# Performance work log

Hardware: AMD Instinct MI355X
Metric: run time of the kernel (lower is better)

Reference implementation:

```python
import jax, jax.numpy as jnp
import numpy as np

N = 100            # node_num
B = 8              # batch
H = 256            # node_feature_hidden_dim
FD, FL = 16, 16    # node_feature_dim, node_feature_len
OUT = 4            # edge_output_dim
E = N * (N - 1)    # 9900 directed edges (off-diagonal)
_off = np.ones((N, N)) - np.eye(N)
REC, SEND = np.where(_off)   # rel_rec one-hot rows = REC, rel_send = SEND
REC = jnp.asarray(REC, jnp.int32)
SEND = jnp.asarray(SEND, jnp.int32)
BN_EPS = 1e-5


def _mlp(x, w1, b1, w2, b2, g, beta):
    # Linear-ReLU-Linear-ReLU-BatchNorm1d (training-mode batch stats, dropout=0)
    h = jax.nn.relu(x @ w1 + b1)
    h = jax.nn.relu(h @ w2 + b2)
    b_, e_, f_ = h.shape
    hf = h.reshape(b_ * e_, f_)
    mu = hf.mean(0)
    var = hf.var(0)  # biased variance, as torch BN uses for normalization
    hn = (hf - mu) * jax.lax.rsqrt(var + BN_EPS) * g + beta
    return hn.reshape(b_, e_, f_)


def _node2edge(x):
    # gather form of rel_send @ x / rel_rec @ x, cat([senders, receivers])
    return jnp.concatenate([x[:, SEND, :], x[:, REC, :]], axis=2)


def _edge2node(x):
    # scatter form of rel_rec.T @ x; original divides by incoming.size(1) == N
    incoming = jnp.zeros((x.shape[0], N, x.shape[2]), x.dtype).at[:, REC, :].add(x)
    return incoming / N


def setup_inputs() -> dict:
    key = jax.random.key(0)
    ks = jax.random.split(key, 40)

    def rn(k, shape, s=0.05):
        return (jax.random.normal(k, shape) * s).astype(jnp.float32)

    inp = {
        'x': rn(ks[0], (B, N, FD, FL), 1.0),
        'h': rn(ks[1], (B, N, 8, 8), 1.0),
        't_nodes': N,
        't_edges': E,
        'nodes_mask': jnp.ones((N,), jnp.int32),
        'edges_mask': jnp.ones((E,), jnp.int32),
    }
    n_in = {'mlp1': FD * FL, 'mlp2': 2 * H, 'mlp3': H, 'mlp4': 3 * H}
    i = 2
    for name, nin in n_in.items():
        inp[name + '_w1'] = rn(ks[i], (nin, H)); i += 1
        inp[name + '_b1'] = jnp.full((H,), 0.1, jnp.float32)
        inp[name + '_w2'] = rn(ks[i], (H, H)); i += 1
        inp[name + '_b2'] = jnp.full((H,), 0.1, jnp.float32)
        inp[name + '_g'] = jnp.ones((H,), jnp.float32)
        inp[name + '_beta'] = jnp.zeros((H,), jnp.float32)
    inp['fc_w'] = rn(ks[i], (H, OUT)); i += 1
    inp['fc_b'] = jnp.full((OUT,), 0.1, jnp.float32)
    return inp


def reference(x, h, t_nodes, t_edges, nodes_mask, edges_mask,
              mlp1_w1, mlp1_b1, mlp1_w2, mlp1_b2, mlp1_g, mlp1_beta,
              mlp2_w1, mlp2_b1, mlp2_w2, mlp2_b2, mlp2_g, mlp2_beta,
              mlp3_w1, mlp3_b1, mlp3_w2, mlp3_b2, mlp3_g, mlp3_beta,
              mlp4_w1, mlp4_b1, mlp4_w2, mlp4_b2, mlp4_g, mlp4_beta,
              fc_w, fc_b):
    # h, t_nodes, t_edges, nodes_mask, edges_mask are unused by the original forward
    xx = x.reshape(x.shape[0], x.shape[1], -1).astype(jnp.float32)  # [B,N,FD*FL]
    xx = _mlp(xx, mlp1_w1, mlp1_b1, mlp1_w2, mlp1_b2, mlp1_g, mlp1_beta)  # [B,N,H]
    xe = _node2edge(xx)                                                   # [B,E,2H]
    xe = _mlp(xe, mlp2_w1, mlp2_b1, mlp2_w2, mlp2_b2, mlp2_g, mlp2_beta)  # [B,E,H]
    x_skip = xe
    xn = _edge2node(xe)                                                   # [B,N,H]
    xn = _mlp(xn, mlp3_w1, mlp3_b1, mlp3_w2, mlp3_b2, mlp3_g, mlp3_beta)
    xe2 = _node2edge(xn)                                                  # [B,E,2H]
    xc = jnp.concatenate([xe2, x_skip], axis=2)                           # [B,E,3H]
    xc = _mlp(xc, mlp4_w1, mlp4_b1, mlp4_w2, mlp4_b2, mlp4_g, mlp4_beta)  # [B,E,H]
    z_g = xc @ fc_w + fc_b                                                # [B,E,OUT]
    return z_g
```

## Files before the change

kernel.cpp:

```cpp
#include <hip/hip_runtime.h>
#include <hip/hip_bf16.h>

#define Nn 100
#define Bb 8
#define Hh 256
#define Ee 9900
#define RE 79200
#define RN 800
#define BN_EPS 1e-5f

typedef __attribute__((ext_vector_type(8))) unsigned short ushort8_t;
typedef __attribute__((ext_vector_type(4))) unsigned short ushort4_t;
typedef __attribute__((ext_vector_type(8))) short bf16x8;
typedef __attribute__((ext_vector_type(4))) float f32x4;

__device__ __forceinline__ float bf2f(unsigned short u){
  return __uint_as_float(((unsigned)u) << 16);
}
__device__ __forceinline__ unsigned short f2bf(float f){
  unsigned u = __float_as_uint(f);
  return (unsigned short)((u + 0x7fffu + ((u >> 16) & 1u)) >> 16);
}

__device__ __forceinline__ void affine_prologue(const float* __restrict__ stats,
    float cnt, const float* __restrict__ g, const float* __restrict__ beta,
    float* a, float* c, int tid){
  if (tid < 256){
    float inv = 1.0f / cnt;
    float mu  = stats[tid] * inv;
    float var = fmaxf(stats[256 + tid] * inv - mu * mu, 0.f);
    float aa  = g[tid] * rsqrtf(var + BN_EPS);
    a[tid] = aa;
    c[tid] = beta[tid] - mu * aa;
  }
}

__device__ __forceinline__ void affine_reg(const float* __restrict__ stats,
    float cnt, const float* __restrict__ g, const float* __restrict__ be,
    int cb, float4& av, float4& cv){
  float4 s = *(const float4*)(stats + cb);
  float4 q = *(const float4*)(stats + 256 + cb);
  float4 gg = *(const float4*)(g + cb);
  float4 bb = *(const float4*)(be + cb);
  float inv = 1.0f / cnt;
  float mx = s.x*inv, my = s.y*inv, mz = s.z*inv, mw = s.w*inv;
  av.x = gg.x * rsqrtf(fmaxf(q.x*inv - mx*mx, 0.f) + BN_EPS); cv.x = bb.x - mx*av.x;
  av.y = gg.y * rsqrtf(fmaxf(q.y*inv - my*my, 0.f) + BN_EPS); cv.y = bb.y - my*av.y;
  av.z = gg.z * rsqrtf(fmaxf(q.z*inv - mz*mz, 0.f) + BN_EPS); cv.z = bb.z - mz*av.z;
  av.w = gg.w * rsqrtf(fmaxf(q.w*inv - mw*mw, 0.f) + BN_EPS); cv.w = bb.w - mw*av.w;
}

__device__ __forceinline__ void gemm_f32(const float* IN, const float* __restrict__ W,
                                         float acc[8][4], int tr, int tc){
  for (int k = 0; k < 256; k += 4){
    float4 w0 = *(const float4*)(W + (size_t)(k+0)*256 + 4*tc);
    float4 w1 = *(const float4*)(W + (size_t)(k+1)*256 + 4*tc);
    float4 w2 = *(const float4*)(W + (size_t)(k+2)*256 + 4*tc);
    float4 w3 = *(const float4*)(W + (size_t)(k+3)*256 + 4*tc);
    #pragma unroll
    for (int rr = 0; rr < 8; rr++){
      float4 iv = *(const float4*)(IN + (tr*8+rr)*256 + k);
      acc[rr][0] += iv.x*w0.x + iv.y*w1.x + iv.z*w2.x + iv.w*w3.x;
      acc[rr][1] += iv.x*w0.y + iv.y*w1.y + iv.z*w2.y + iv.w*w3.y;
      acc[rr][2] += iv.x*w0.z + iv.y*w1.z + iv.z*w2.z + iv.w*w3.z;
      acc[rr][3] += iv.x*w0.w + iv.y*w1.w + iv.z*w2.w + iv.w*w3.w;
    }
  }
}

__device__ __forceinline__ void mfma_gemm64(const unsigned short* Alds,
    const unsigned short* __restrict__ Bf, f32x4 acc[4][4], int w, int lane){
  const int l15 = lane & 15, kg = lane >> 4;
  for (int ks = 0; ks < 8; ks++){
    bf16x8 a[4];
    #pragma unroll
    for (int rf = 0; rf < 4; rf++){
      int byte = (((rf*16 + l15)*256 + ks*32 + kg*8) * 2) ^ ((l15 & 7) << 4);
      a[rf] = *(const bf16x8*)((const char*)Alds + byte);
    }
    const unsigned short* bp = Bf + ((size_t)(ks*16 + w*4)*64 + lane)*8;
    #pragma unroll
    for (int cf = 0; cf < 4; cf++){
      bf16x8 b = *(const bf16x8*)(bp + cf*64*8);
      #pragma unroll
      for (int rf = 0; rf < 4; rf++)
        acc[rf][cf] = __builtin_amdgcn_mfma_f32_16x16x32_bf16(a[rf], b, acc[rf][cf], 0,0,0);
    }
  }
}

__device__ __forceinline__ void zero_acc4(f32x4 acc[4][4]){
  #pragma unroll
  for (int i = 0; i < 4; i++)
    #pragma unroll
    for (int j = 0; j < 4; j++){
      f32x4 z = {0.f, 0.f, 0.f, 0.f};
      acc[i][j] = z;
    }
}

#define STATS_PUSH(statsp)                                   \
  __syncthreads();                                           \
  atomicAdd(&(statsp)[tid], red[tid]);                       \
  atomicAdd(&(statsp)[tid + 256], red[tid + 256]);

__global__ void k_wprep(const float* __restrict__ W, unsigned short* __restrict__ out,
                        int ktiles){
  int id = blockIdx.x * 256 + threadIdx.x;
  int total = ktiles * 16 * 64;
  if (id >= total) return;
  int lane = id & 63, tile = id >> 6;
  int tc = tile & 15, tk = tile >> 4;
  int kbase = tk*32 + (lane>>4)*8, col = tc*16 + (lane&15);
  ushort8_t o;
  #pragma unroll
  for (int j = 0; j < 8; j++) o[j] = f2bf(W[(size_t)(kbase+j)*256 + col]);
  *(ushort8_t*)(out + (size_t)id*8) = o;
}

__global__ __launch_bounds__(256,2) void k_mlp1(
    const float* __restrict__ x,
    const float* __restrict__ W1, const float* __restrict__ b1,
    const float* __restrict__ W2, const float* __restrict__ b2,
    float* __restrict__ h1, float* __restrict__ stats){
  __shared__ float IN[32*256];
  __shared__ float O1[32*256];
  __shared__ float red[512];
  int tid = threadIdx.x, tr = tid >> 6, tc = tid & 63;
  int r0 = blockIdx.x * 32;
  #pragma unroll
  for (int j = 0; j < 8; j++){
    int idx = tid*4 + j*1024;
    *(float4*)(IN + idx) = *(const float4*)(x + (size_t)r0*256 + idx);
  }
  red[tid] = 0.f; red[tid + 256] = 0.f;
  __syncthreads();
  float acc[8][4];
  #pragma unroll
  for (int rr = 0; rr < 8; rr++){ acc[rr][0]=acc[rr][1]=acc[rr][2]=acc[rr][3]=0.f; }
  gemm_f32(IN, W1, acc, tr, tc);
  {
    float4 bb = *(const float4*)(b1 + 4*tc);
    #pragma unroll
    for (int rr = 0; rr < 8; rr++){
      float4 o;
      o.x = fmaxf(acc[rr][0]+bb.x, 0.f);
      o.y = fmaxf(acc[rr][1]+bb.y, 0.f);
      o.z = fmaxf(acc[rr][2]+bb.z, 0.f);
      o.w = fmaxf(acc[rr][3]+bb.w, 0.f);
      *(float4*)(O1 + (tr*8+rr)*256 + 4*tc) = o;
    }
  }
  __syncthreads();
  #pragma unroll
  for (int rr = 0; rr < 8; rr++){ acc[rr][0]=acc[rr][1]=acc[rr][2]=acc[rr][3]=0.f; }
  gemm_f32(O1, W2, acc, tr, tc);
  {
    float4 bb = *(const float4*)(b2 + 4*tc);
    float ls0=0,ls1=0,ls2=0,ls3=0,lq0=0,lq1=0,lq2=0,lq3=0;
    #pragma unroll
    for (int rr = 0; rr < 8; rr++){
      float4 v;
      v.x = fmaxf(acc[rr][0]+bb.x, 0.f);
      v.y = fmaxf(acc[rr][1]+bb.y, 0.f);
      v.z = fmaxf(acc[rr][2]+bb.z, 0.f);
      v.w = fmaxf(acc[rr][3]+bb.w, 0.f);
      *(float4*)(h1 + ((size_t)(r0 + tr*8 + rr))*256 + 4*tc) = v;
      ls0+=v.x; lq0+=v.x*v.x; ls1+=v.y; lq1+=v.y*v.y;
      ls2+=v.z; lq2+=v.z*v.z; ls3+=v.w; lq3+=v.w*v.w;
    }
    atomicAdd(&red[4*tc+0], ls0); atomicAdd(&red[4*tc+1], ls1);
    atomicAdd(&red[4*tc+2], ls2); atomicAdd(&red[4*tc+3], ls3);
    atomicAdd(&red[256+4*tc+0], lq0); atomicAdd(&red[256+4*tc+1], lq1);
    atomicAdd(&red[256+4*tc+2], lq2); atomicAdd(&red[256+4*tc+3], lq3);
  }
  STATS_PUSH(stats)
}

__global__ __launch_bounds__(256,2) void k_nodepq(
    const float* __restrict__ hsrc, const float* __restrict__ stats,
    const float* __restrict__ g, const float* __restrict__ be,
    const float* __restrict__ W512,
    unsigned short* __restrict__ P, unsigned short* __restrict__ Q){
  __shared__ float IN[32*256];
  int tid = threadIdx.x, tr = tid >> 6, tc = tid & 63;
  int part = blockIdx.x / 25;
  int r0 = (blockIdx.x % 25) * 32;
  int cb = (tid*4) & 255;
  float4 av, cv;
  affine_reg(stats, (float)RN, g, be, cb, av, cv);
  #pragma unroll
  for (int j = 0; j < 8; j++){
    int idx = tid*4 + j*1024;
    int row = idx >> 8;
    float4 v = *(const float4*)(hsrc + (size_t)(r0+row)*256 + cb);
    float4 o;
    o.x = v.x*av.x + cv.x; o.y = v.y*av.y + cv.y;
    o.z = v.z*av.z + cv.z; o.w = v.w*av.w + cv.w;
    *(float4*)(IN + idx) = o;
  }
  __syncthreads();
  float acc[8][4];
  #pragma unroll
  for (int rr = 0; rr < 8; rr++){ acc[rr][0]=acc[rr][1]=acc[rr][2]=acc[rr][3]=0.f; }
  gemm_f32(IN, W512 + (size_t)part*65536, acc, tr, tc);
  unsigned short* out = part ? Q : P;
  #pragma unroll
  for (int rr = 0; rr < 8; rr++){
    ushort4_t o;
    o[0]=f2bf(acc[rr][0]); o[1]=f2bf(acc[rr][1]);
    o[2]=f2bf(acc[rr][2]); o[3]=f2bf(acc[rr][3]);
    *(ushort4_t*)(out + (size_t)(r0 + tr*8 + rr)*256 + 4*tc) = o;
  }
}

__global__ __launch_bounds__(256,4) void k_mlp2(
    const unsigned short* __restrict__ P2, const unsigned short* __restrict__ Q2,
    const float* __restrict__ b1,
    const unsigned short* __restrict__ W2f, const float* __restrict__ b2,
    unsigned short* __restrict__ h2, float* __restrict__ stats2){
  __shared__ unsigned short O1[64*256];
  __shared__ float red[512];
  int tid = threadIdx.x, w = tid >> 6, lane = tid & 63;
  int l15 = lane & 15, kg = lane >> 4;
  int r0 = blockIdx.x * 64;
  red[tid] = 0.f; red[tid + 256] = 0.f;
  {
    int cb = lane * 4;
    float4 bb = *(const float4*)(b1 + cb);
    #pragma unroll
    for (int rr = 0; rr < 16; rr++){
      int rl = w*16+rr, rg = r0 + rl;
      int rgc = rg < RE ? rg : RE-1;
      int b = rgc / Ee, e = rgc - b*Ee;
      int i = e / 99, kk = e - i*99;
      int snd = kk + (kk >= i);
      ushort4_t pv = *(const ushort4_t*)(P2 + ((size_t)(b*Nn + snd))*256 + cb);
      ushort4_t qv = *(const ushort4_t*)(Q2 + ((size_t)(b*Nn + i))*256 + cb);
      ushort4_t o;
      o[0] = f2bf(fmaxf(bf2f(pv[0])+bf2f(qv[0])+bb.x, 0.f));
      o[1] = f2bf(fmaxf(bf2f(pv[1])+bf2f(qv[1])+bb.y, 0.f));
      o[2] = f2bf(fmaxf(bf2f(pv[2])+bf2f(qv[2])+bb.z, 0.f));
      o[3] = f2bf(fmaxf(bf2f(pv[3])+bf2f(qv[3])+bb.w, 0.f));
      int byte = ((rl*256 + cb)*2) ^ ((rl&7)<<4);
      *(ushort4_t*)((char*)O1 + byte) = o;
    }
  }
  __syncthreads();
  f32x4 acc2[4][4];
  zero_acc4(acc2);
  mfma_gemm64(O1, W2f, acc2, w, lane);
  {
    #pragma unroll
    for (int cf = 0; cf < 4; cf++){
      int col = w*64 + cf*16 + l15;
      float bb = b2[col];
      float ls = 0.f, lq = 0.f;
      #pragma unroll
      for (int rf = 0; rf < 4; rf++){
        #pragma unroll
        for (int r = 0; r < 4; r++){
          int row = rf*16 + kg*4 + r;
          if (r0 + row < RE){
            float v = fmaxf(acc2[rf][cf][r] + bb, 0.f);
            h2[(size_t)(r0 + row)*256 + col] = f2bf(v);
            ls += v; lq += v*v;
          }
        }
      }
      atomicAdd(&red[col], ls);
      atomicAdd(&red[256+col], lq);
    }
  }
  STATS_PUSH(stats2)
}

__global__ __launch_bounds__(256,4) void k_e2n(
    const unsigned short* __restrict__ h2, float* __restrict__ h3in){
  int m = blockIdx.x;
  int b = m / Nn, i = m - b*Nn;
  int c = threadIdx.x;
  const unsigned short* base = h2 + ((size_t)(b*Ee + i*99))*256 + c;
  float s = 0.f;
  #pragma unroll 4
  for (int j = 0; j < 99; j++) s += bf2f(base[(size_t)j*256]);
  h3in[(size_t)m*256 + c] = s;
}

__global__ __launch_bounds__(256,2) void k_mlp3(
    const float* __restrict__ h3in, const float* __restrict__ stats2,
    const float* __restrict__ g2, const float* __restrict__ be2,
    const float* __restrict__ W1, const float* __restrict__ b1,
    const float* __restrict__ W2, const float* __restrict__ b2,
    float* __restrict__ h3, float* __restrict__ stats3){
  __shared__ float IN[32*256];
  __shared__ float O1[32*256];
  __shared__ float red[512];
  __shared__ float ap[256], cp[256];
  int tid = threadIdx.x, tr = tid >> 6, lane = tid & 63, tc = lane;
  int r0 = blockIdx.x * 32;
  affine_prologue(stats2, (float)RE, g2, be2, ap, cp, tid);
  red[tid] = 0.f; red[tid + 256] = 0.f;
  __syncthreads();
  {
    int cb = lane * 4;
    float4 av = *(const float4*)(ap+cb), cv = *(const float4*)(cp+cb);
    #pragma unroll
    for (int rr = 0; rr < 8; rr++){
      int m = r0 + tr*8 + rr;
      float4 s = *(const float4*)(h3in + (size_t)m*256 + cb);
      float4 o;
      o.x = (s.x*av.x + 99.f*cv.x) * 0.01f;
      o.y = (s.y*av.y + 99.f*cv.y) * 0.01f;
      o.z = (s.z*av.z + 99.f*cv.z) * 0.01f;
      o.w = (s.w*av.w + 99.f*cv.w) * 0.01f;
      *(float4*)(IN + (tr*8+rr)*256 + cb) = o;
    }
  }
  __syncthreads();
  float acc[8][4];
  #pragma unroll
  for (int rr = 0; rr < 8; rr++){ acc[rr][0]=acc[rr][1]=acc[rr][2]=acc[rr][3]=0.f; }
  gemm_f32(IN, W1, acc, tr, tc);
  {
    float4 bb = *(const float4*)(b1 + 4*tc);
    #pragma unroll
    for (int rr = 0; rr < 8; rr++){
      float4 o;
      o.x = fmaxf(acc[rr][0]+bb.x, 0.f);
      o.y = fmaxf(acc[rr][1]+bb.y, 0.f);
      o.z = fmaxf(acc[rr][2]+bb.z, 0.f);
      o.w = fmaxf(acc[rr][3]+bb.w, 0.f);
      *(float4*)(O1 + (tr*8+rr)*256 + 4*tc) = o;
    }
  }
  __syncthreads();
  #pragma unroll
  for (int rr = 0; rr < 8; rr++){ acc[rr][0]=acc[rr][1]=acc[rr][2]=acc[rr][3]=0.f; }
  gemm_f32(O1, W2, acc, tr, tc);
  {
    float4 bb = *(const float4*)(b2 + 4*tc);
    float ls0=0,ls1=0,ls2=0,ls3=0,lq0=0,lq1=0,lq2=0,lq3=0;
    #pragma unroll
    for (int rr = 0; rr < 8; rr++){
      float4 v;
      v.x = fmaxf(acc[rr][0]+bb.x, 0.f);
      v.y = fmaxf(acc[rr][1]+bb.y, 0.f);
      v.z = fmaxf(acc[rr][2]+bb.z, 0.f);
      v.w = fmaxf(acc[rr][3]+bb.w, 0.f);
      *(float4*)(h3 + ((size_t)(r0 + tr*8 + rr))*256 + 4*tc) = v;
      ls0+=v.x; lq0+=v.x*v.x; ls1+=v.y; lq1+=v.y*v.y;
      ls2+=v.z; lq2+=v.z*v.z; ls3+=v.w; lq3+=v.w*v.w;
    }
    atomicAdd(&red[4*tc+0], ls0); atomicAdd(&red[4*tc+1], ls1);
    atomicAdd(&red[4*tc+2], ls2); atomicAdd(&red[4*tc+3], ls3);
    atomicAdd(&red[256+4*tc+0], lq0); atomicAdd(&red[256+4*tc+1], lq1);
    atomicAdd(&red[256+4*tc+2], lq2); atomicAdd(&red[256+4*tc+3], lq3);
  }
  STATS_PUSH(stats3)
}

__global__ __launch_bounds__(256,4) void k_mlp4(
    const unsigned short* __restrict__ h2,
    const float* __restrict__ stats2, const float* __restrict__ g2, const float* __restrict__ be2,
    const unsigned short* __restrict__ P4, const unsigned short* __restrict__ Q4,
    const float* __restrict__ b1,
    const unsigned short* __restrict__ Wsf,
    const unsigned short* __restrict__ W2f, const float* __restrict__ b2,
    unsigned short* __restrict__ h4, float* __restrict__ stats4){
  __shared__ unsigned short A[64*256];
  __shared__ float red[512];
  __shared__ int sIdx[64], rIdx[64];
  int tid = threadIdx.x, w = tid >> 6, lane = tid & 63;
  int l15 = lane & 15, kg = lane >> 4;
  int r0 = blockIdx.x * 64;
  red[tid] = 0.f; red[tid + 256] = 0.f;
  if (tid < 64){
    int rg = r0 + tid;
    int rgc = rg < RE ? rg : RE-1;
    int b = rgc / Ee, e = rgc - b*Ee;
    int i = e / 99, kk = e - i*99;
    int snd = kk + (kk >= i);
    sIdx[tid] = (b*Nn + snd)*256;
    rIdx[tid] = (b*Nn + i)*256;
  }
  {
    int cb = lane * 4;
    float4 av, cv;
    affine_reg(stats2, (float)RE, g2, be2, cb, av, cv);
    #pragma unroll
    for (int rr = 0; rr < 16; rr++){
      int rl = w*16+rr, rg = r0 + rl;
      int rgc = rg < RE ? rg : RE-1;
      ushort4_t hv = *(const ushort4_t*)(h2 + (size_t)rgc*256 + cb);
      ushort4_t o;
      o[0]=f2bf(bf2f(hv[0])*av.x+cv.x);
      o[1]=f2bf(bf2f(hv[1])*av.y+cv.y);
      o[2]=f2bf(bf2f(hv[2])*av.z+cv.z);
      o[3]=f2bf(bf2f(hv[3])*av.w+cv.w);
      int byte = ((rl*256 + cb)*2) ^ ((rl&7)<<4);
      *(ushort4_t*)((char*)A + byte) = o;
    }
  }
  __syncthreads();
  f32x4 acc[4][4];
  zero_acc4(acc);
  mfma_gemm64(A, Wsf, acc, w, lane);
  __syncthreads();
  unsigned short* O1 = A;
  {
    #pragma unroll
    for (int cf = 0; cf < 4; cf++){
      int col = w*64 + cf*16 + l15;
      float bb = b1[col];
      #pragma unroll
      for (int rf = 0; rf < 4; rf++){
        #pragma unroll
        for (int r = 0; r < 4; r++){
          int row = rf*16 + kg*4 + r;
          float v = acc[rf][cf][r] + bf2f(P4[sIdx[row] + col]) + bf2f(Q4[rIdx[row] + col]) + bb;
          v = fmaxf(v, 0.f);
          int byte = ((row*256 + col)*2) ^ ((row&7)<<4);
          *(unsigned short*)((char*)O1 + byte) = f2bf(v);
        }
      }
    }
  }
  __syncthreads();
  f32x4 acc2[4][4];
  zero_acc4(acc2);
  mfma_gemm64(O1, W2f, acc2, w, lane);
  {
    #pragma unroll
    for (int cf = 0; cf < 4; cf++){
      int col = w*64 + cf*16 + l15;
      float bb = b2[col];
      float ls = 0.f, lq = 0.f;
      #pragma unroll
      for (int rf = 0; rf < 4; rf++){
        #pragma unroll
        for (int r = 0; r < 4; r++){
          int row = rf*16 + kg*4 + r;
          if (r0 + row < RE){
            float v = fmaxf(acc2[rf][cf][r] + bb, 0.f);
            h4[(size_t)(r0 + row)*256 + col] = f2bf(v);
            ls += v; lq += v*v;
          }
        }
      }
      atomicAdd(&red[col], ls);
      atomicAdd(&red[256+col], lq);
    }
  }
  STATS_PUSH(stats4)
}

__global__ __launch_bounds__(256,2) void k_out(
    const unsigned short* __restrict__ h4, const float* __restrict__ stats4,
    const float* __restrict__ g4, const float* __restrict__ be4,
    const float* __restrict__ fcw, const float* __restrict__ fcb,
    float* __restrict__ out){
  __shared__ unsigned short T[64*264];
  __shared__ float a4[256], c4[256], Wl[1024];
  int tid = threadIdx.x;
  affine_prologue(stats4, (float)RE, g4, be4, a4, c4, tid);
  #pragma unroll
  for (int j = 0; j < 4; j++){ int id = tid + j*256; Wl[id] = fcw[id]; }
  int r0 = blockIdx.x * 64;
  #pragma unroll
  for (int j = 0; j < 8; j++){
    int flat = tid + j*256;
    int rl = flat >> 5, cs = (flat & 31) * 8;
    ushort8_t v = {0,0,0,0,0,0,0,0};
    if (r0 + rl < RE) v = *(const ushort8_t*)(h4 + (size_t)(r0+rl)*256 + cs);
    *(ushort8_t*)(&T[rl*264 + cs]) = v;
  }
  __syncthreads();
  int row = tid >> 2, o = tid & 3;
  if (r0 + row < RE){
    float acc = fcb[o];
    for (int k = 0; k < 256; k += 8){
      ushort8_t iv = *(const ushort8_t*)(&T[row*264 + k]);
      #pragma unroll
      for (int kk = 0; kk < 8; kk++){
        float v = bf2f(iv[kk]) * a4[k+kk] + c4[k+kk];
        acc += v * Wl[(k+kk)*4 + o];
      }
    }
    out[(size_t)(r0+row)*4 + o] = acc;
  }
}

extern "C" void kernel_launch(void* const* d_in, const int* in_sizes, int n_in,
                              void* d_out, int out_size, void* d_ws, size_t ws_size,
                              hipStream_t stream){
  const float* x    = (const float*)d_in[0];
  const float* m1w1 = (const float*)d_in[6];  const float* m1b1 = (const float*)d_in[7];
  const float* m1w2 = (const float*)d_in[8];  const float* m1b2 = (const float*)d_in[9];
  const float* m1g  = (const float*)d_in[10]; const float* m1be = (const float*)d_in[11];
  const float* m2w1 = (const float*)d_in[12]; const float* m2b1 = (const float*)d_in[13];
  const float* m2w2 = (const float*)d_in[14]; const float* m2b2 = (const float*)d_in[15];
  const float* m2g  = (const float*)d_in[16]; const float* m2be = (const float*)d_in[17];
  const float* m3w1 = (const float*)d_in[18]; const float* m3b1 = (const float*)d_in[19];
  const float* m3w2 = (const float*)d_in[20]; const float* m3b2 = (const float*)d_in[21];
  const float* m3g  = (const float*)d_in[22]; const float* m3be = (const float*)d_in[23];
  const float* m4w1 = (const float*)d_in[24]; const float* m4b1 = (const float*)d_in[25];
  const float* m4w2 = (const float*)d_in[26]; const float* m4b2 = (const float*)d_in[27];
  const float* m4g  = (const float*)d_in[28]; const float* m4be = (const float*)d_in[29];
  const float* fcw  = (const float*)d_in[30]; const float* fcb  = (const float*)d_in[31];

  size_t need_bytes = 616448ull * 4ull
                    + (2ull * (size_t)RE * 256ull + 3ull * 65536ull + 4ull * 204800ull) * 2ull;
  if (ws_size < need_bytes) return;

  float* ws = (float*)d_ws;
  float* h1   = ws;
  float* h3   = ws + 204800;
  float* stats= ws + 409600;
  float* h3in = ws + 411648;
  unsigned short* h2  = (unsigned short*)(ws + 616448);
  unsigned short* h4  = h2 + (size_t)RE * 256;
  unsigned short* w2b = h4 + (size_t)RE * 256;
  unsigned short* w4s = w2b + 65536;
  unsigned short* w4b = w4s + 65536;
  unsigned short* P2b = w4b + 65536;
  unsigned short* Q2b = P2b + 204800;
  unsigned short* P4b = Q2b + 204800;
  unsigned short* Q4b = P4b + 204800;

  hipMemsetAsync(stats, 0, 2048 * sizeof(float), stream);

  k_wprep<<<(8*16*64)/256, 256, 0, stream>>>(m2w2, w2b, 8);
  k_wprep<<<(8*16*64)/256, 256, 0, stream>>>(m4w1 + (size_t)512*256, w4s, 8);
  k_wprep<<<(8*16*64)/256, 256, 0, stream>>>(m4w2, w4b, 8);

  k_mlp1<<<RN/32, 256, 0, stream>>>(x, m1w1, m1b1, m1w2, m1b2, h1, stats);
  k_nodepq<<<50, 256, 0, stream>>>(h1, stats, m1g, m1be, m2w1, P2b, Q2b);
  k_mlp2<<<(RE+63)/64, 256, 0, stream>>>(P2b, Q2b, m2b1, w2b, m2b2, h2, stats + 512);
  k_e2n<<<RN, 256, 0, stream>>>(h2, h3in);
  k_mlp3<<<RN/32, 256, 0, stream>>>(h3in, stats + 512, m2g, m2be,
                                    m3w1, m3b1, m3w2, m3b2, h3, stats + 1024);
  k_nodepq<<<50, 256, 0, stream>>>(h3, stats + 1024, m3g, m3be, m4w1, P4b, Q4b);
  k_mlp4<<<(RE+63)/64, 256, 0, stream>>>(h2, stats + 512, m2g, m2be,
                                         P4b, Q4b, m4b1, w4s, w4b, m4b2, h4, stats + 1536);
  k_out<<<(RE+63)/64, 256, 0, stream>>>(h4, stats + 1536, m4g, m4be,
                                        fcw, fcb, (float*)d_out);
}
```

Measured before the change: 504.7 us.

## Stage MLP outputs through LDS for coalesced stores, prefetch P/Q gathers, merge weight prep

In the edge MLP kernels, the second-GEMM outputs are written to swizzled shared memory first and then stored to global memory as 16-byte row-contiguous vectors, replacing scattered 2-byte stores. In k_mlp4 the P4/Q4 gather-sum is precomputed cooperatively with vector loads into shared memory before the epilogue, so the epilogue no longer issues scalar indirect global loads. The three weight-prep launches are merged into one kernel. This adds extra barriers and LDS traffic in exchange for better coalescing.

```diff
diff --git a/kernel.cpp b/kernel.cpp
--- a/kernel.cpp
+++ b/kernel.cpp
@@ -104,11 +104,13 @@
   atomicAdd(&(statsp)[tid], red[tid]);                       \
   atomicAdd(&(statsp)[tid + 256], red[tid + 256]);
 
-__global__ void k_wprep(const float* __restrict__ W, unsigned short* __restrict__ out,
-                        int ktiles){
-  int id = blockIdx.x * 256 + threadIdx.x;
-  int total = ktiles * 16 * 64;
-  if (id >= total) return;
+__global__ void k_wprep3(const float* __restrict__ Wa, unsigned short* __restrict__ Oa,
+                         const float* __restrict__ Wb, unsigned short* __restrict__ Ob,
+                         const float* __restrict__ Wc, unsigned short* __restrict__ Oc){
+  int gid = blockIdx.x * 256 + threadIdx.x;
+  int seg = gid >> 13, id = gid & 8191;
+  const float* W = seg == 0 ? Wa : (seg == 1 ? Wb : Wc);
+  unsigned short* out = seg == 0 ? Oa : (seg == 1 ? Ob : Oc);
   int lane = id & 63, tile = id >> 6;
   int tc = tile & 15, tk = tile >> 4;
   int kbase = tk*32 + (lane>>4)*8, col = tc*16 + (lane&15);
@@ -250,6 +252,7 @@
   f32x4 acc2[4][4];
   zero_acc4(acc2);
   mfma_gemm64(O1, W2f, acc2, w, lane);
+  __syncthreads();
   {
     #pragma unroll
     for (int cf = 0; cf < 4; cf++){
@@ -261,15 +264,27 @@
         #pragma unroll
         for (int r = 0; r < 4; r++){
           int row = rf*16 + kg*4 + r;
-          if (r0 + row < RE){
-            float v = fmaxf(acc2[rf][cf][r] + bb, 0.f);
-            h2[(size_t)(r0 + row)*256 + col] = f2bf(v);
-            ls += v; lq += v*v;
-          }
+          float v = fmaxf(acc2[rf][cf][r] + bb, 0.f);
+          int byte = ((row*256 + col)*2) ^ ((row&7)<<4);
+          *(unsigned short*)((char*)O1 + byte) = f2bf(v);
+          if (r0 + row < RE){ ls += v; lq += v*v; }
         }
       }
       atomicAdd(&red[col], ls);
       atomicAdd(&red[256+col], lq);
+    }
+  }
+  __syncthreads();
+  {
+    #pragma unroll
+    for (int p = 0; p < 8; p++){
+      int flat = tid + p*256;
+      int rl = flat >> 5, cs = (flat & 31) * 8;
+      if (r0 + rl < RE){
+        int byte = ((rl*256 + cs)*2) ^ ((rl&7)<<4);
+        ushort8_t v = *(const ushort8_t*)((const char*)O1 + byte);
+        *(ushort8_t*)(h2 + (size_t)(r0+rl)*256 + cs) = v;
+      }
     }
   }
   STATS_PUSH(stats2)
@@ -407,7 +422,40 @@
   zero_acc4(acc);
   mfma_gemm64(A, Wsf, acc, w, lane);
   __syncthreads();
-  unsigned short* O1 = A;
+  {
+    int cb = lane * 4;
+    #pragma unroll
+    for (int rr = 0; rr < 16; rr++){
+      int rl = w*16+rr;
+      ushort4_t pv = *(const ushort4_t*)(P4 + sIdx[rl] + cb);
+      ushort4_t qv = *(const ushort4_t*)(Q4 + rIdx[rl] + cb);
+      ushort4_t o;
+      o[0]=f2bf(bf2f(pv[0])+bf2f(qv[0]));
+      o[1]=f2bf(bf2f(pv[1])+bf2f(qv[1]));
+      o[2]=f2bf(bf2f(pv[2])+bf2f(qv[2]));
+      o[3]=f2bf(bf2f(pv[3])+bf2f(qv[3]));
+      int byte = ((rl*256 + cb)*2) ^ ((rl&7)<<4);
+      *(ushort4_t*)((char*)A + byte) = o;
+    }
+  }
+  __syncthreads();
+  ushort4_t pqr[4][4];
+  #pragma unroll
+  for (int cf = 0; cf < 4; cf++){
+    int col = w*64 + cf*16 + l15;
+    #pragma unroll
+    for (int rf = 0; rf < 4; rf++){
+      ushort4_t t;
+      #pragma unroll
+      for (int r = 0; r < 4; r++){
+        int row = rf*16 + kg*4 + r;
+        int byte = ((row*256 + col)*2) ^ ((row&7)<<4);
+        t[r] = *(const unsigned short*)((const char*)A + byte);
+      }
+      pqr[cf][rf] = t;
+    }
+  }
+  __syncthreads();
   {
     #pragma unroll
     for (int cf = 0; cf < 4; cf++){
@@ -418,10 +466,9 @@
         #pragma unroll
         for (int r = 0; r < 4; r++){
           int row = rf*16 + kg*4 + r;
-          float v = acc[rf][cf][r] + bf2f(P4[sIdx[row] + col]) + bf2f(Q4[rIdx[row] + col]) + bb;
-          v = fmaxf(v, 0.f);
+          float v = fmaxf(acc[rf][cf][r] + bf2f(pqr[cf][rf][r]) + bb, 0.f);
           int byte = ((row*256 + col)*2) ^ ((row&7)<<4);
-          *(unsigned short*)((char*)O1 + byte) = f2bf(v);
+          *(unsigned short*)((char*)A + byte) = f2bf(v);
         }
       }
     }
@@ -429,7 +476,8 @@
   __syncthreads();
   f32x4 acc2[4][4];
   zero_acc4(acc2);
-  mfma_gemm64(O1, W2f, acc2, w, lane);
+  mfma_gemm64(A, W2f, acc2, w, lane);
+  __syncthreads();
   {
     #pragma unroll
     for (int cf = 0; cf < 4; cf++){
@@ -441,15 +489,27 @@
         #pragma unroll
         for (int r = 0; r < 4; r++){
           int row = rf*16 + kg*4 + r;
-          if (r0 + row < RE){
-            float v = fmaxf(acc2[rf][cf][r] + bb, 0.f);
-            h4[(size_t)(r0 + row)*256 + col] = f2bf(v);
-            ls += v; lq += v*v;
-          }
+          float v = fmaxf(acc2[rf][cf][r] + bb, 0.f);
+          int byte = ((row*256 + col)*2) ^ ((row&7)<<4);
+          *(unsigned short*)((char*)A + byte) = f2bf(v);
+          if (r0 + row < RE){ ls += v; lq += v*v; }
         }
       }
       atomicAdd(&red[col], ls);
       atomicAdd(&red[256+col], lq);
+    }
+  }
+  __syncthreads();
+  {
+    #pragma unroll
+    for (int p = 0; p < 8; p++){
+      int flat = tid + p*256;
+      int rl = flat >> 5, cs = (flat & 31) * 8;
+      if (r0 + rl < RE){
+        int byte = ((rl*256 + cs)*2) ^ ((rl&7)<<4);
+        ushort8_t v = *(const ushort8_t*)((const char*)A + byte);
+        *(ushort8_t*)(h4 + (size_t)(r0+rl)*256 + cs) = v;
+      }
     }
   }
   STATS_PUSH(stats4)
@@ -530,9 +590,7 @@
 
   hipMemsetAsync(stats, 0, 2048 * sizeof(float), stream);
 
-  k_wprep<<<(8*16*64)/256, 256, 0, stream>>>(m2w2, w2b, 8);
-  k_wprep<<<(8*16*64)/256, 256, 0, stream>>>(m4w1 + (size_t)512*256, w4s, 8);
-  k_wprep<<<(8*16*64)/256, 256, 0, stream>>>(m4w2, w4b, 8);
+  k_wprep3<<<96, 256, 0, stream>>>(m2w2, w2b, m4w1 + (size_t)512*256, w4s, m4w2, w4b);
 
   k_mlp1<<<RN/32, 256, 0, stream>>>(x, m1w1, m1b1, m1w2, m1b2, h1, stats);
   k_nodepq<<<50, 256, 0, stream>>>(h1, stats, m1g, m1be, m2w1, P2b, Q2b);
```

Result: slower. 529.7 us (+4.9%).
